# Performance work log

Measured on AMD Instinct MI355X. Metric: run time of the kernel, lower is better.

## Reference

```python
import jax, jax.numpy as jnp
import numpy as np

B, N, C = 64, 196, 768
H = 12
HD = C // H            # 64
TOPK = int(0.25 * HD)  # 16
HIDDEN = int(C * 4.0)  # 3072
SCALE = HD ** -0.5
EPS = 1e-5


def layernorm(x, g, b):
    mu = jnp.mean(x, axis=-1, keepdims=True)
    var = jnp.var(x, axis=-1, keepdims=True)
    return (x - mu) * jax.lax.rsqrt(var + EPS) * g + b


def setup_inputs() -> dict:
    key = jax.random.key(0)
    ks = jax.random.split(key, 8)
    s = 0.02
    return {
        "x": jax.random.normal(ks[0], (B, N, C), jnp.float32),
        "norm1_g": jnp.ones((C,), jnp.float32),
        "norm1_b": jnp.zeros((C,), jnp.float32),
        "qk_w": jax.random.normal(ks[1], (2 * C, C), jnp.float32) * s,   # torch Linear [out,in], no bias
        "attn_proj_w": jax.random.normal(ks[2], (C, H * TOPK), jnp.float32) * s,
        "attn_proj_b": jnp.zeros((C,), jnp.float32),
        "norm2_g": jnp.ones((C,), jnp.float32),
        "norm2_b": jnp.zeros((C,), jnp.float32),
        "fc1_w": jax.random.normal(ks[3], (HIDDEN, C), jnp.float32) * s,
        "fc1_b": jnp.zeros((HIDDEN,), jnp.float32),
        "fc2_w": jax.random.normal(ks[4], (C, HIDDEN), jnp.float32) * s,
        "fc2_b": jnp.zeros((C,), jnp.float32),
    }


def reference(x, norm1_g, norm1_b, qk_w, attn_proj_w, attn_proj_b,
              norm2_g, norm2_b, fc1_w, fc1_b, fc2_w, fc2_b):
    # --- HomoAttention branch ---
    h = layernorm(x, norm1_g, norm1_b)                       # [B,N,C]
    qk = h @ qk_w.T                                          # [B,N,2C]
    qk = qk.reshape(B, N, 2, H, HD).transpose(2, 0, 3, 1, 4) # [2,B,H,N,HD]
    q, k = qk[0] * SCALE, qk[1]
    attn = jnp.einsum('bhnd,bhmd->bhnm', q, k)               # [B,H,N,N]
    top_vals, _ = jax.lax.top_k(attn, TOPK)                  # [B,H,N,TOPK]
    a = jax.nn.softmax(top_vals, axis=-1)
    a = a.transpose(0, 2, 1, 3).reshape(B, N, H * TOPK)      # [B,N,H*TOPK]
    x = x + a @ attn_proj_w.T + attn_proj_b

    # --- MLP branch ---
    h2 = layernorm(x, norm2_g, norm2_b)
    h2 = jax.nn.gelu(h2 @ fc1_w.T + fc1_b, approximate=False)
    x = x + h2 @ fc2_w.T + fc2_b
    return x
```

## Files before the change

### kernel.cpp

```cpp
#include <hip/hip_runtime.h>


#define BATCH 64
#define SEQ   196
#define CH    768
#define NHEAD 12
#define HDIM  64
#define TOPK  16
#define HID   3072
#define MROWS 12544
#define MHALF 6272
#define SCALE_F 0.125f
#define NEGBIG -3e38f

typedef __bf16 bf16x8 __attribute__((ext_vector_type(8)));
typedef float  f32x4  __attribute__((ext_vector_type(4)));

__device__ __forceinline__ unsigned short f2b(float f) {
    union { float f; unsigned int i; } c; c.f = f;
    unsigned int u = c.i;
    return (unsigned short)((u + 0x7fffu + ((u >> 16) & 1u)) >> 16);
}
__device__ __forceinline__ float b2f(unsigned short u) {
    union { unsigned int i; float f; } c; c.i = ((unsigned int)u) << 16; return c.f;
}

__device__ __forceinline__ float gelu_f(float v) {
    float u = v * (0.7978845608f + 0.0356774081f * v * v);
    float e = __expf(2.0f * u);
    float th = 1.0f - 2.0f / (e + 1.0f);
    return 0.5f * v * (1.0f + th);
}

__device__ __forceinline__ void async16(const unsigned short* g, unsigned short* l) {
    __builtin_amdgcn_global_load_lds(
        (const __attribute__((address_space(1))) unsigned int*)(g),
        (__attribute__((address_space(3))) unsigned int*)(l), 16, 0, 0);
}

__global__ __launch_bounds__(256) void f2b4_k(const float* __restrict__ s0, unsigned short* __restrict__ d0, int n0,
                                              const float* __restrict__ s1, unsigned short* __restrict__ d1, int n1,
                                              const float* __restrict__ s2, unsigned short* __restrict__ d2, int n2,
                                              const float* __restrict__ s3, unsigned short* __restrict__ d3, int n3)
{
    int idx = (blockIdx.x * 256 + threadIdx.x) * 4;
    const float* s; unsigned short* d; int n;
    if (idx < n0) { s = s0; d = d0; n = n0; }
    else {
        idx -= n0;
        if (idx < n1) { s = s1; d = d1; n = n1; }
        else {
            idx -= n1;
            if (idx < n2) { s = s2; d = d2; n = n2; }
            else { idx -= n2; s = s3; d = d3; n = n3; }
        }
    }
    if (idx < n) {
        float4 v = *(const float4*)(s + idx);
        ushort4 o;
        o.x = f2b(v.x); o.y = f2b(v.y); o.z = f2b(v.z); o.w = f2b(v.w);
        *(ushort4*)(d + idx) = o;
    }
}

template<bool INF32>
__global__ __launch_bounds__(256) void ln_k(const void* __restrict__ xin,
                                            const float* __restrict__ gw,
                                            const float* __restrict__ bw,
                                            unsigned short* __restrict__ out)
{
    const int row = blockIdx.x;
    const int tid = threadIdx.x;
    float v0, v1, v2;
    if constexpr (INF32) {
        const float* xr = (const float*)xin + (size_t)row * CH;
        v0 = xr[tid]; v1 = xr[tid + 256]; v2 = xr[tid + 512];
    } else {
        const unsigned short* xr = (const unsigned short*)xin + (size_t)row * CH;
        v0 = b2f(xr[tid]); v1 = b2f(xr[tid + 256]); v2 = b2f(xr[tid + 512]);
    }
    float s  = v0 + v1 + v2;
    float sq = v0*v0 + v1*v1 + v2*v2;
#pragma unroll
    for (int off = 32; off > 0; off >>= 1) {
        s  += __shfl_down(s, off, 64);
        sq += __shfl_down(sq, off, 64);
    }
    __shared__ __align__(16) float red[8];
    if ((tid & 63) == 0) { red[(tid >> 6) * 2] = s; red[(tid >> 6) * 2 + 1] = sq; }
    __syncthreads();
    s  = red[0] + red[2] + red[4] + red[6];
    sq = red[1] + red[3] + red[5] + red[7];
    float mu  = s * (1.0f / CH);
    float var = sq * (1.0f / CH) - mu * mu;
    float rs  = rsqrtf(var + 1e-5f);
    unsigned short* orow = out + (size_t)row * CH;
    orow[tid]       = f2b((v0 - mu) * rs * gw[tid]       + bw[tid]);
    orow[tid + 256] = f2b((v1 - mu) * rs * gw[tid + 256] + bw[tid + 256]);
    orow[tid + 512] = f2b((v2 - mu) * rs * gw[tid + 512] + bw[tid + 512]);
}

template<int TM, int TN, bool BIAS, int RES, bool GELU, bool OUTF>
__global__ __launch_bounds__(256, 4)
void gemm_bt(const unsigned short* __restrict__ A,
             const unsigned short* __restrict__ Bw,
             const float* __restrict__ bias,
             const void* __restrict__ resid,
             void* __restrict__ Cout,
             int M, int N, int K)
{
    constexpr int WROWS = (TM == 128) ? 2 : 1;
    constexpr int WCOLS = 4 / WROWS;
    constexpr int JF = TN / (16 * WCOLS);
    __shared__ __align__(16) unsigned short As[2][TM * 32];
    __shared__ __align__(16) unsigned short Bs[2][TN * 32];
    const int tid  = threadIdx.x;
    const int w    = tid >> 6;
    const int lane = tid & 63;

    const int gridN = gridDim.x, gridM = gridDim.y;
    const int lid = blockIdx.y * gridN + blockIdx.x;
    const int SG = 8 * gridN;
    const int sg = lid / SG, r = lid % SG;
    const int remM = gridM - sg * 8;
    int mloc, nloc;
    if (remM >= 8) { mloc = sg * 8 + (r & 7); nloc = r >> 3; }
    else           { mloc = sg * 8 + r % remM; nloc = r / remM; }
    const int tileM = mloc * TM;
    const int tileN = nloc * TN;

    const int wm = (w / WCOLS) * 64;
    const int wn = (w % WCOLS) * (JF * 16);
    const int q   = lane >> 4;
    const int l16 = lane & 15;
    const int csw = (q ^ (l16 & 3)) * 8;

    f32x4 acc[4][JF];
#pragma unroll
    for (int i = 0; i < 4; ++i)
#pragma unroll
        for (int j = 0; j < JF; ++j) acc[i][j] = (f32x4){0.f, 0.f, 0.f, 0.f};

    const int r0 = tid >> 2;
    const int g0 = ((tid & 3) ^ (r0 & 3)) * 8;

    const unsigned short* pB[TN / 64];
    const unsigned short* pA[TM / 64];
#pragma unroll
    for (int c = 0; c < TN / 64; ++c) pB[c] = Bw + (size_t)(tileN + r0 + c * 64) * K + g0;
#pragma unroll
    for (int c = 0; c < TM / 64; ++c) pA[c] = A + (size_t)(tileM + r0 + c * 64) * K + g0;

    auto stage = [&](int buf) {
#pragma unroll
        for (int c = 0; c < TN / 64; ++c) {
            async16(pB[c], &Bs[buf][(size_t)(c * 256 + w * 64) * 8]);
            pB[c] += 32;
        }
#pragma unroll
        for (int c = 0; c < TM / 64; ++c) {
            async16(pA[c], &As[buf][(size_t)(c * 256 + w * 64) * 8]);
            pA[c] += 32;
        }
    };

    const int kIters = K >> 5;
    stage(0);
    int cur = 0;
    for (int kt = 0; kt < kIters; ++kt) {
        __syncthreads();
        if (kt + 1 < kIters) stage(cur ^ 1);
        bf16x8 af[4], bfr[JF];
#pragma unroll
        for (int i = 0; i < 4; ++i)
            af[i] = *(const bf16x8*)&As[cur][(wm + i * 16 + l16) * 32 + csw];
#pragma unroll
        for (int j = 0; j < JF; ++j)
            bfr[j] = *(const bf16x8*)&Bs[cur][(wn + j * 16 + l16) * 32 + csw];
#pragma unroll
        for (int i = 0; i < 4; ++i)
#pragma unroll
            for (int j = 0; j < JF; ++j)
                acc[i][j] = __builtin_amdgcn_mfma_f32_16x16x32_bf16(af[i], bfr[j], acc[i][j], 0, 0, 0);
        cur ^= 1;
    }

#pragma unroll
    for (int i = 0; i < 4; ++i) {
#pragma unroll
        for (int r2 = 0; r2 < 4; ++r2) {
            int row = tileM + wm + i * 16 + q * 4 + r2;
#pragma unroll
            for (int j = 0; j < JF; ++j) {
                int col = tileN + wn + j * 16 + l16;
                float v = acc[i][j][r2];
                if (BIAS) v += bias[col];
                if (GELU) v = gelu_f(v);
                if (RES == 1) v += ((const float*)resid)[(size_t)row * N + col];
                if (RES == 2) v += b2f(((const unsigned short*)resid)[(size_t)row * N + col]);
                if (OUTF) ((float*)Cout)[(size_t)row * N + col] = v;
                else      ((unsigned short*)Cout)[(size_t)row * N + col] = f2b(v);
            }
        }
    }
}

__global__ __launch_bounds__(256) void attn_topk(const unsigned short* __restrict__ qk,
                                                 unsigned short* __restrict__ aout)
{
    const int bh = blockIdx.x;
    const int b = bh / NHEAD, h = bh % NHEAD;
    __shared__ __align__(16) unsigned short Qs[208 * 64];
    __shared__ __align__(16) unsigned short Ks[208 * 64];
    const int tid = threadIdx.x;

    for (int i = tid; i < 208 * 8; i += 256) {
        int row = i >> 3, c = i & 7;
        uint4 vq = make_uint4(0, 0, 0, 0), vk = vq;
        if (row < SEQ) {
            const uint4* gp = (const uint4*)(qk + ((size_t)(b * SEQ + row) * 1536 + h * 64));
            vq = gp[c];
            vk = gp[c + 96];
        }
        int slot = c ^ (row & 7);
        *(uint4*)&Qs[row * 64 + slot * 8] = vq;
        *(uint4*)&Ks[row * 64 + slot * 8] = vk;
    }
    __syncthreads();

    const int w = tid >> 6, lane = tid & 63;
    const int q = lane >> 4, l16 = lane & 15;

    for (int tn = w; tn < 13; tn += 4) {
        const int nrow = tn * 16 + l16;
        const int nsw = nrow & 7;
        bf16x8 bq0 = *(const bf16x8*)&Qs[nrow * 64 + ((0 * 4 + q) ^ nsw) * 8];
        bf16x8 bq1 = *(const bf16x8*)&Qs[nrow * 64 + ((1 * 4 + q) ^ nsw) * 8];

        float t[TOPK];
#pragma unroll
        for (int j = 0; j < TOPK; ++j) t[j] = NEGBIG;

        for (int tm = 0; tm < 12; ++tm) {
            const int mrow = tm * 16 + l16;
            const int msw = mrow & 7;
            bf16x8 ak0 = *(const bf16x8*)&Ks[mrow * 64 + ((0 * 4 + q) ^ msw) * 8];
            bf16x8 ak1 = *(const bf16x8*)&Ks[mrow * 64 + ((1 * 4 + q) ^ msw) * 8];
            f32x4 acc = (f32x4){0.f, 0.f, 0.f, 0.f};
            acc = __builtin_amdgcn_mfma_f32_16x16x32_bf16(ak0, bq0, acc, 0, 0, 0);
            acc = __builtin_amdgcn_mfma_f32_16x16x32_bf16(ak1, bq1, acc, 0, 0, 0);
#pragma unroll
            for (int r = 0; r < 4; ++r) {
                float v = acc[r];
#pragma unroll
                for (int j = 0; j < TOPK; ++j) {
                    float mx = fmaxf(t[j], v);
                    v = fminf(t[j], v);
                    t[j] = mx;
                }
            }
        }
        {
            const int mrow = 12 * 16 + l16;
            const int msw = mrow & 7;
            bf16x8 ak0 = *(const bf16x8*)&Ks[mrow * 64 + ((0 * 4 + q) ^ msw) * 8];
            bf16x8 ak1 = *(const bf16x8*)&Ks[mrow * 64 + ((1 * 4 + q) ^ msw) * 8];
            f32x4 acc = (f32x4){0.f, 0.f, 0.f, 0.f};
            acc = __builtin_amdgcn_mfma_f32_16x16x32_bf16(ak0, bq0, acc, 0, 0, 0);
            acc = __builtin_amdgcn_mfma_f32_16x16x32_bf16(ak1, bq1, acc, 0, 0, 0);
#pragma unroll
            for (int r = 0; r < 4; ++r) {
                float v = (q == 0) ? acc[r] : NEGBIG;
#pragma unroll
                for (int j = 0; j < TOPK; ++j) {
                    float mx = fmaxf(t[j], v);
                    v = fminf(t[j], v);
                    t[j] = mx;
                }
            }
        }

#pragma unroll
        for (int stage = 0; stage < 2; ++stage) {
            const int xm = 16 << stage;
            float bl[TOPK], c[TOPK];
#pragma unroll
            for (int j = 0; j < TOPK; ++j) bl[j] = __shfl_xor(t[j], xm, 64);
#pragma unroll
            for (int j = 0; j < TOPK; ++j) c[j] = fmaxf(t[j], bl[TOPK - 1 - j]);
#pragma unroll
            for (int s = 8; s >= 1; s >>= 1) {
#pragma unroll
                for (int i = 0; i < TOPK; ++i) {
                    if ((i & s) == 0) {
                        float mx = fmaxf(c[i], c[i + s]);
                        c[i + s] = fminf(c[i], c[i + s]);
                        c[i] = mx;
                    }
                }
            }
#pragma unroll
            for (int j = 0; j < TOPK; ++j) t[j] = c[j];
        }

        if (q == 0 && nrow < SEQ) {
            float e[TOPK], sum = 0.f;
#pragma unroll
            for (int j = 0; j < TOPK; ++j) { e[j] = __expf((t[j] - t[0]) * SCALE_F); sum += e[j]; }
            float inv = 1.0f / sum;
            unsigned int pk[8];
#pragma unroll
            for (int jj = 0; jj < 8; ++jj)
                pk[jj] = (unsigned int)f2b(e[2 * jj] * inv) |
                         ((unsigned int)f2b(e[2 * jj + 1] * inv) << 16);
            unsigned short* dst = aout + ((size_t)(b * SEQ + nrow)) * (NHEAD * TOPK) + h * TOPK;
            ((uint4*)dst)[0] = make_uint4(pk[0], pk[1], pk[2], pk[3]);
            ((uint4*)dst)[1] = make_uint4(pk[4], pk[5], pk[6], pk[7]);
        }
    }
}

extern "C" void kernel_launch(void* const* d_in, const int* in_sizes, int n_in,
                              void* d_out, int out_size, void* d_ws, size_t ws_size,
                              hipStream_t stream)
{
    const float* x    = (const float*)d_in[0];
    const float* g1   = (const float*)d_in[1];
    const float* bb1  = (const float*)d_in[2];
    const float* qkw  = (const float*)d_in[3];
    const float* pw   = (const float*)d_in[4];
    const float* pb   = (const float*)d_in[5];
    const float* g2   = (const float*)d_in[6];
    const float* bb2  = (const float*)d_in[7];
    const float* f1w  = (const float*)d_in[8];
    const float* f1b  = (const float*)d_in[9];
    const float* f2w  = (const float*)d_in[10];
    const float* f2bp = (const float*)d_in[11];
    float* out = (float*)d_out;

    char* ws = (char*)d_ws;
    const size_t SZ_H   = (size_t)MROWS * CH * 2;
    const size_t N_WQK  = (size_t)2 * CH * CH;
    const size_t N_WP   = (size_t)CH * (NHEAD * TOPK);
    const size_t N_WF   = (size_t)HID * CH;
    const size_t SZ_W   = (N_WQK + N_WP + 2 * N_WF) * 2;
    const size_t SZ_A   = (size_t)MROWS * (NHEAD * TOPK) * 2;
    const size_t SZ_QK  = (size_t)MROWS * 2 * CH * 2;
    const size_t SZ_GGF = (size_t)MROWS * HID * 2;

    unsigned short* hbuf = (unsigned short*)(ws);
    unsigned short* wqk  = (unsigned short*)(ws + SZ_H);
    unsigned short* wp   = wqk + N_WQK;
    unsigned short* wf1  = wp  + N_WP;
    unsigned short* wf2  = wf1 + N_WF;
    unsigned short* av   = (unsigned short*)(ws + SZ_H + SZ_W);
    unsigned short* qk   = (unsigned short*)(ws + SZ_H + SZ_W + SZ_A);
    unsigned short* gg   = qk;

    const size_t base = SZ_H + SZ_W + SZ_A;
    const bool fullMLP = ws_size >= base + SZ_GGF + SZ_H;
    const bool bx1     = fullMLP || ws_size >= base + SZ_QK + SZ_H;
    unsigned short* x1b = (unsigned short*)(ws + base + (fullMLP ? SZ_GGF : SZ_QK));
    float* x1 = out;

    {
        int total4 = (int)((N_WQK + N_WP + 2 * N_WF) / 4);
        f2b4_k<<<(total4 + 255) / 256, 256, 0, stream>>>(
            qkw, wqk, (int)N_WQK, pw, wp, (int)N_WP,
            f1w, wf1, (int)N_WF, f2w, wf2, (int)N_WF);
    }

    ln_k<true><<<MROWS, 256, 0, stream>>>(x, g1, bb1, hbuf);
    gemm_bt<128, 128, false, 0, false, false><<<dim3(12, 98), 256, 0, stream>>>(
        hbuf, wqk, nullptr, nullptr, qk, MROWS, 2*CH, CH);
    attn_topk<<<BATCH * NHEAD, 256, 0, stream>>>(qk, av);

    if (bx1) {
        gemm_bt<64, 128, true, 1, false, false><<<dim3(6, 196), 256, 0, stream>>>(
            av, wp, pb, x, x1b, MROWS, CH, NHEAD*TOPK);
        ln_k<false><<<MROWS, 256, 0, stream>>>(x1b, g2, bb2, hbuf);
        if (fullMLP) {
            gemm_bt<128, 128, true, 0, true, false><<<dim3(24, 98), 256, 0, stream>>>(
                hbuf, wf1, f1b, nullptr, gg, MROWS, HID, CH);
            gemm_bt<64, 256, true, 2, false, true><<<dim3(3, 196), 256, 0, stream>>>(
                gg, wf2, f2bp, x1b, out, MROWS, CH, HID);
        } else {
            for (int half = 0; half < 2; ++half) {
                const size_t ro = (size_t)half * MHALF;
                gemm_bt<128, 128, true, 0, true, false><<<dim3(24, 49), 256, 0, stream>>>(
                    hbuf + ro * CH, wf1, f1b, nullptr, gg, MHALF, HID, CH);
                gemm_bt<64, 256, true, 2, false, true><<<dim3(3, 98), 256, 0, stream>>>(
                    gg, wf2, f2bp, x1b + ro * CH, out + ro * CH, MHALF, CH, HID);
            }
        }
    } else {
        gemm_bt<64, 128, true, 1, false, true><<<dim3(6, 196), 256, 0, stream>>>(
            av, wp, pb, x, x1, MROWS, CH, NHEAD*TOPK);
        ln_k<true><<<MROWS, 256, 0, stream>>>(x1, g2, bb2, hbuf);
        for (int half = 0; half < 2; ++half) {
            const size_t ro = (size_t)half * MHALF;
            gemm_bt<128, 128, true, 0, true, false><<<dim3(24, 49), 256, 0, stream>>>(
                hbuf + ro * CH, wf1, f1b, nullptr, gg, MHALF, HID, CH);
            gemm_bt<64, 256, true, 1, false, true><<<dim3(3, 98), 256, 0, stream>>>(
                gg, wf2, f2bp, x1 + ro * CH, out + ro * CH, MHALF, CH, HID);
        }
    }
}
```

Baseline: 438.6 us.

## Add 256x256 eight-wave pipelined GEMM for QK, FC1 and FC2 projections

Introduces a new bf16 MFMA GEMM kernel with 256x256 output tiles, 512 threads, double-buffered async global-to-LDS staging split into quarter stages interleaved with MFMA phases, setprio hints, and a grouped tile ordering for L2 reuse. It replaces the 128x128 and 64x256 GEMMs for the QK projection and both MLP GEMMs on the full-workspace path. The larger tiles cut global traffic per FLOP. In exchange, register and LDS use rise, and there are fewer tiles to spread across the compute units. MROWS=12544 divides evenly by 256 (49 tiles), so no bounds checks are needed.

Result: slower. 448.6 us (+2.3%).

```diff
diff --git a/kernel.cpp b/kernel.cpp
--- a/kernel.cpp
+++ b/kernel.cpp
@@ -205,6 +205,178 @@
     }
 }
 
+template<int KC, bool BIAS, int RES, bool GELU, bool OUTF>
+__global__ __launch_bounds__(512, 2)
+void gemm8p(const unsigned short* __restrict__ A,
+            const unsigned short* __restrict__ Bw,
+            const float* __restrict__ bias,
+            const void* __restrict__ resid,
+            void* __restrict__ Cout,
+            int M, int N)
+{
+    constexpr int T = KC / 64;
+    __shared__ __align__(16) unsigned short As[2][256 * 64];
+    __shared__ __align__(16) unsigned short Bs[2][256 * 64];
+    const int tid  = threadIdx.x;
+    const int w    = tid >> 6;
+    const int lane = tid & 63;
+    const int q    = lane >> 4;
+    const int l16  = lane & 15;
+
+    const int gridN = gridDim.x, gridM = gridDim.y;
+    const int lid = blockIdx.y * gridN + blockIdx.x;
+    const int SG = 8 * gridN;
+    const int sg = lid / SG, rr = lid % SG;
+    const int remM = gridM - sg * 8;
+    int mloc, nloc;
+    if (remM >= 8) { mloc = sg * 8 + (rr & 7); nloc = rr >> 3; }
+    else           { mloc = sg * 8 + rr % remM; nloc = rr / remM; }
+    const int tileM = mloc * 256, tileN = nloc * 256;
+
+    const int wm = (w >> 2) * 128;
+    const int wn = (w & 3) * 64;
+
+    const int r0 = tid >> 3;
+    const int g0 = (tid & 7) ^ (r0 & 7);
+    const unsigned short* pA0 = A  + (size_t)(tileM + r0) * KC + g0 * 8;
+    const unsigned short* pB0 = Bw + (size_t)(tileN + r0) * KC + g0 * 8;
+
+    auto stageHT = [&](int v, int j) {
+        const unsigned short* src = (j < 2 ? pA0 : pB0)
+                                  + (size_t)(j & 1) * 128 * KC + (size_t)v * 64;
+        unsigned short* dst = (j < 2 ? As[v & 1] : Bs[v & 1]) + (j & 1) * 8192 + w * 512;
+        async16(src, dst);
+        async16(src + (size_t)64 * KC, dst + 4096);
+    };
+
+    f32x4 acc[8][4];
+#pragma unroll
+    for (int i = 0; i < 8; ++i)
+#pragma unroll
+        for (int jn = 0; jn < 4; ++jn) acc[i][jn] = (f32x4){0.f, 0.f, 0.f, 0.f};
+
+    stageHT(0, 0); stageHT(0, 1); stageHT(0, 2); stageHT(0, 3); stageHT(1, 0);
+    asm volatile("s_waitcnt vmcnt(2)" ::: "memory");
+    __builtin_amdgcn_s_barrier();
+
+    const int arow = wm + l16;
+    const int brow = wn + l16;
+    const int xsw  = l16 & 7;
+
+#pragma unroll 2
+    for (int u = 0; u < T; ++u) {
+        const unsigned short* Ab = As[u & 1];
+        const unsigned short* Bb = Bs[u & 1];
+        bf16x8 af[4][2], b0[2][2], b1[2][2];
+
+#pragma unroll
+        for (int m = 0; m < 4; ++m)
+#pragma unroll
+            for (int kk = 0; kk < 2; ++kk)
+                af[m][kk] = *(const bf16x8*)&Ab[(arow + m * 16) * 64 + ((((kk << 2) | q) ^ xsw) << 3)];
+#pragma unroll
+        for (int n = 0; n < 2; ++n)
+#pragma unroll
+            for (int kk = 0; kk < 2; ++kk)
+                b0[n][kk] = *(const bf16x8*)&Bb[(brow + n * 16) * 64 + ((((kk << 2) | q) ^ xsw) << 3)];
+        if (u + 1 < T) stageHT(u + 1, 1);
+        __builtin_amdgcn_s_barrier();
+        asm volatile("s_waitcnt lgkmcnt(0)" ::: "memory");
+        __builtin_amdgcn_sched_barrier(0);
+        __builtin_amdgcn_s_setprio(1);
+#pragma unroll
+        for (int kk = 0; kk < 2; ++kk)
+#pragma unroll
+            for (int m = 0; m < 4; ++m)
+#pragma unroll
+                for (int n = 0; n < 2; ++n)
+                    acc[m][n] = __builtin_amdgcn_mfma_f32_16x16x32_bf16(af[m][kk], b0[n][kk], acc[m][n], 0, 0, 0);
+        __builtin_amdgcn_s_setprio(0);
+        __builtin_amdgcn_s_barrier();
+
+#pragma unroll
+        for (int n = 0; n < 2; ++n)
+#pragma unroll
+            for (int kk = 0; kk < 2; ++kk)
+                b1[n][kk] = *(const bf16x8*)&Bb[(brow + 32 + n * 16) * 64 + ((((kk << 2) | q) ^ xsw) << 3)];
+        if (u + 1 < T) stageHT(u + 1, 2);
+        __builtin_amdgcn_s_barrier();
+        asm volatile("s_waitcnt lgkmcnt(0)" ::: "memory");
+        __builtin_amdgcn_sched_barrier(0);
+        __builtin_amdgcn_s_setprio(1);
+#pragma unroll
+        for (int kk = 0; kk < 2; ++kk)
+#pragma unroll
+            for (int m = 0; m < 4; ++m)
+#pragma unroll
+                for (int n = 0; n < 2; ++n)
+                    acc[m][2 + n] = __builtin_amdgcn_mfma_f32_16x16x32_bf16(af[m][kk], b1[n][kk], acc[m][2 + n], 0, 0, 0);
+        __builtin_amdgcn_s_setprio(0);
+        __builtin_amdgcn_s_barrier();
+
+#pragma unroll
+        for (int m = 0; m < 4; ++m)
+#pragma unroll
+            for (int kk = 0; kk < 2; ++kk)
+                af[m][kk] = *(const bf16x8*)&Ab[(arow + 64 + m * 16) * 64 + ((((kk << 2) | q) ^ xsw) << 3)];
+        if (u + 1 < T) stageHT(u + 1, 3);
+        __builtin_amdgcn_s_barrier();
+        asm volatile("s_waitcnt lgkmcnt(0)" ::: "memory");
+        __builtin_amdgcn_sched_barrier(0);
+        __builtin_amdgcn_s_setprio(1);
+#pragma unroll
+        for (int kk = 0; kk < 2; ++kk)
+#pragma unroll
+            for (int m = 0; m < 4; ++m)
+#pragma unroll
+                for (int n = 0; n < 2; ++n)
+                    acc[4 + m][2 + n] = __builtin_amdgcn_mfma_f32_16x16x32_bf16(af[m][kk], b1[n][kk], acc[4 + m][2 + n], 0, 0, 0);
+        __builtin_amdgcn_s_setprio(0);
+        __builtin_amdgcn_s_barrier();
+
+        if (u + 2 < T) {
+            stageHT(u + 2, 0);
+            asm volatile("s_waitcnt vmcnt(2)" ::: "memory");
+        } else if (u + 1 < T) {
+            asm volatile("s_waitcnt vmcnt(0)" ::: "memory");
+        }
+        __builtin_amdgcn_s_barrier();
+        __builtin_amdgcn_s_setprio(1);
+#pragma unroll
+        for (int kk = 0; kk < 2; ++kk)
+#pragma unroll
+            for (int m = 0; m < 4; ++m)
+#pragma unroll
+                for (int n = 0; n < 2; ++n)
+                    acc[4 + m][n] = __builtin_amdgcn_mfma_f32_16x16x32_bf16(af[m][kk], b0[n][kk], acc[4 + m][n], 0, 0, 0);
+        __builtin_amdgcn_s_setprio(0);
+        __builtin_amdgcn_s_barrier();
+    }
+
+#pragma unroll
+    for (int mh = 0; mh < 2; ++mh)
+#pragma unroll
+        for (int m = 0; m < 4; ++m)
+#pragma unroll
+            for (int r2 = 0; r2 < 4; ++r2) {
+                const int row = tileM + wm + mh * 64 + m * 16 + q * 4 + r2;
+#pragma unroll
+                for (int nh = 0; nh < 2; ++nh)
+#pragma unroll
+                    for (int n = 0; n < 2; ++n) {
+                        const int col = tileN + wn + nh * 32 + n * 16 + l16;
+                        float v = acc[mh * 4 + m][nh * 2 + n][r2];
+                        if (BIAS) v += bias[col];
+                        if (GELU) v = gelu_f(v);
+                        if (RES == 1) v += ((const float*)resid)[(size_t)row * N + col];
+                        if (RES == 2) v += b2f(((const unsigned short*)resid)[(size_t)row * N + col]);
+                        if (OUTF) ((float*)Cout)[(size_t)row * N + col] = v;
+                        else      ((unsigned short*)Cout)[(size_t)row * N + col] = f2b(v);
+                    }
+            }
+    (void)M;
+}
+
 __global__ __launch_bounds__(256) void attn_topk(const unsigned short* __restrict__ qk,
                                                  unsigned short* __restrict__ aout)
 {
@@ -371,19 +543,19 @@
     }
 
     ln_k<true><<<MROWS, 256, 0, stream>>>(x, g1, bb1, hbuf);
-    gemm_bt<128, 128, false, 0, false, false><<<dim3(12, 98), 256, 0, stream>>>(
-        hbuf, wqk, nullptr, nullptr, qk, MROWS, 2*CH, CH);
+    gemm8p<CH, false, 0, false, false><<<dim3(2 * CH / 256, MROWS / 256), 512, 0, stream>>>(
+        hbuf, wqk, nullptr, nullptr, qk, MROWS, 2 * CH);
     attn_topk<<<BATCH * NHEAD, 256, 0, stream>>>(qk, av);
 
     if (bx1) {
         gemm_bt<64, 128, true, 1, false, false><<<dim3(6, 196), 256, 0, stream>>>(
-            av, wp, pb, x, x1b, MROWS, CH, NHEAD*TOPK);
+            av, wp, pb, x, x1b, MROWS, CH, NHEAD * TOPK);
         ln_k<false><<<MROWS, 256, 0, stream>>>(x1b, g2, bb2, hbuf);
         if (fullMLP) {
-            gemm_bt<128, 128, true, 0, true, false><<<dim3(24, 98), 256, 0, stream>>>(
-                hbuf, wf1, f1b, nullptr, gg, MROWS, HID, CH);
-            gemm_bt<64, 256, true, 2, false, true><<<dim3(3, 196), 256, 0, stream>>>(
-                gg, wf2, f2bp, x1b, out, MROWS, CH, HID);
+            gemm8p<CH, true, 0, true, false><<<dim3(HID / 256, MROWS / 256), 512, 0, stream>>>(
+                hbuf, wf1, f1b, nullptr, gg, MROWS, HID);
+            gemm8p<HID, true, 2, false, true><<<dim3(CH / 256, MROWS / 256), 512, 0, stream>>>(
+                gg, wf2, f2bp, x1b, out, MROWS, CH);
         } else {
             for (int half = 0; half < 2; ++half) {
                 const size_t ro = (size_t)half * MHALF;
@@ -395,7 +567,7 @@
         }
     } else {
         gemm_bt<64, 128, true, 1, false, true><<<dim3(6, 196), 256, 0, stream>>>(
-            av, wp, pb, x, x1, MROWS, CH, NHEAD*TOPK);
+            av, wp, pb, x, x1, MROWS, CH, NHEAD * TOPK);
         ln_k<true><<<MROWS, 256, 0, stream>>>(x1, g2, bb2, hbuf);
         for (int half = 0; half < 2; ++half) {
             const size_t ro = (size_t)half * MHALF;
```

## Replace GEMMs with persistent 128x256 tile kernel using LDS-staged vector epilogue

Applied to the files above, without the earlier changes.

Adds a persistent GEMM kernel launched with 768 blocks of 512 threads. Each block walks 128x256 output tiles in an order grouped by M so blocks share weight panels, with double-buffered async loads over K-slices of 32. The epilogue stages each wave's results in shared memory so global stores are 16-byte vectors. It replaces the QK, projection, FC1 and FC2 GEMMs on the main path, aiming for better B reuse, fewer launches' worth of tail effects and more coalesced writes. It assumes M is a multiple of 128 and N a multiple of 256, and uses larger shared-memory buffers that may lower occupancy.

New measurement: 433.4 us. About the same (-1.2%).

```diff
diff --git a/kernel.cpp b/kernel.cpp
--- a/kernel.cpp
+++ b/kernel.cpp
@@ -205,6 +205,159 @@
     }
 }
 
+template<bool BIAS, int RES, bool GELU, bool OUTF>
+__global__ __launch_bounds__(512, 4)
+void gemm_p(const unsigned short* __restrict__ A,
+            const unsigned short* __restrict__ Bw,
+            const float* __restrict__ bias,
+            const void* __restrict__ resid,
+            void* __restrict__ Cout,
+            int M, int N, int K)
+{
+    __shared__ __align__(16) unsigned short As[2][128 * 32];
+    __shared__ __align__(16) unsigned short Bs[2][256 * 32];
+    const int tid  = threadIdx.x;
+    const int w    = tid >> 6;
+    const int lane = tid & 63;
+    const int q    = lane >> 4;
+    const int l16  = lane & 15;
+
+    const int gridM = M >> 7, gridN = N >> 8;
+    const int P = gridDim.x;
+
+    const int x   = (int)blockIdx.x & 7;
+    const int bj  = (int)blockIdx.x >> 3;
+    const int Bx  = (P >> 3) + (((P & 7) > x) ? 1 : 0);
+    const int cnt = (gridM - x + 7) >> 3;
+    const int ntx = cnt * gridN;
+
+    const int wm = (w >> 2) * 64;
+    const int wn = (w & 3) * 64;
+    const int r0 = tid >> 2;
+    const int g0 = ((tid & 3) ^ (r0 & 3)) * 8;
+    const int csw = (q ^ (l16 & 3)) * 8;
+
+    for (int t = bj; t < ntx; t += Bx) {
+        const int nn = t / cnt, ii = t - nn * cnt;
+        const int tileM = (x + (ii << 3)) << 7;
+        const int tileN = nn << 8;
+
+        __syncthreads();
+
+        const unsigned short* pA  = A  + (size_t)(tileM + r0) * K + g0;
+        const unsigned short* pB0 = Bw + (size_t)(tileN + r0) * K + g0;
+        const unsigned short* pB1 = Bw + (size_t)(tileN + 128 + r0) * K + g0;
+
+        f32x4 acc[4][4];
+#pragma unroll
+        for (int i = 0; i < 4; ++i)
+#pragma unroll
+            for (int j = 0; j < 4; ++j) acc[i][j] = (f32x4){0.f, 0.f, 0.f, 0.f};
+
+        auto stage = [&](int buf) {
+            async16(pB0, &Bs[buf][(size_t)w * 512]);        pB0 += 32;
+            async16(pB1, &Bs[buf][4096 + (size_t)w * 512]); pB1 += 32;
+            async16(pA,  &As[buf][(size_t)w * 512]);        pA  += 32;
+        };
+
+        const int kIters = K >> 5;
+        stage(0);
+        int cur = 0;
+        for (int kt = 0; kt < kIters; ++kt) {
+            __syncthreads();
+            if (kt + 1 < kIters) stage(cur ^ 1);
+            bf16x8 af[4], bf[4];
+#pragma unroll
+            for (int i = 0; i < 4; ++i)
+                af[i] = *(const bf16x8*)&As[cur][(wm + i * 16 + l16) * 32 + csw];
+#pragma unroll
+            for (int j = 0; j < 4; ++j)
+                bf[j] = *(const bf16x8*)&Bs[cur][(wn + j * 16 + l16) * 32 + csw];
+#pragma unroll
+            for (int i = 0; i < 4; ++i)
+#pragma unroll
+                for (int j = 0; j < 4; ++j)
+                    acc[i][j] = __builtin_amdgcn_mfma_f32_16x16x32_bf16(af[i], bf[j], acc[i][j], 0, 0, 0);
+            cur ^= 1;
+        }
+
+        __syncthreads();
+
+        float bsh[4];
+        if (BIAS) {
+#pragma unroll
+            for (int j = 0; j < 4; ++j) bsh[j] = bias[tileN + wn + j * 16 + l16];
+        }
+
+        if constexpr (!OUTF) {
+            unsigned short* slab = &Bs[0][0] + (size_t)w * 1152;
+            unsigned short* co = (unsigned short*)Cout;
+#pragma unroll
+            for (int i = 0; i < 4; ++i) {
+#pragma unroll
+                for (int j = 0; j < 4; ++j)
+#pragma unroll
+                    for (int r2 = 0; r2 < 4; ++r2) {
+                        float v = acc[i][j][r2];
+                        if (BIAS) v += bsh[j];
+                        if (GELU) v = gelu_f(v);
+                        slab[(q * 4 + r2) * 72 + j * 16 + l16] = f2b(v);
+                    }
+#pragma unroll
+                for (int h = 0; h < 2; ++h) {
+                    const int lr = h * 8 + (lane >> 3);
+                    const int grow = tileM + wm + i * 16 + lr;
+                    const int gcol = tileN + wn + (lane & 7) * 8;
+                    uint4 pk = *(const uint4*)&slab[lr * 72 + (lane & 7) * 8];
+                    if (RES != 0) {
+                        unsigned short* ps = (unsigned short*)&pk;
+#pragma unroll
+                        for (int jj = 0; jj < 8; ++jj) {
+                            float v = b2f(ps[jj]);
+                            if (RES == 1) v += ((const float*)resid)[(size_t)grow * N + gcol + jj];
+                            if (RES == 2) v += b2f(((const unsigned short*)resid)[(size_t)grow * N + gcol + jj]);
+                            ps[jj] = f2b(v);
+                        }
+                    }
+                    *(uint4*)&co[(size_t)grow * N + gcol] = pk;
+                }
+            }
+        } else {
+            float* slabf = (w == 7) ? (float*)&As[0][0]
+                                    : (float*)&Bs[0][0] + (size_t)w * 1088;
+            float* co = (float*)Cout;
+#pragma unroll
+            for (int i = 0; i < 4; ++i) {
+#pragma unroll
+                for (int j = 0; j < 4; ++j)
+#pragma unroll
+                    for (int r2 = 0; r2 < 4; ++r2) {
+                        float v = acc[i][j][r2];
+                        if (BIAS) v += bsh[j];
+                        if (GELU) v = gelu_f(v);
+                        slabf[(q * 4 + r2) * 68 + j * 16 + l16] = v;
+                    }
+#pragma unroll
+                for (int i4 = 0; i4 < 4; ++i4) {
+                    const int lr = i4 * 4 + (lane >> 4);
+                    const int grow = tileM + wm + i * 16 + lr;
+                    const int gcol = tileN + wn + (lane & 15) * 4;
+                    f32x4 vv = *(const f32x4*)&slabf[lr * 68 + (lane & 15) * 4];
+                    if (RES == 1) {
+                        const float4 r4 = *(const float4*)&((const float*)resid)[(size_t)grow * N + gcol];
+                        vv[0] += r4.x; vv[1] += r4.y; vv[2] += r4.z; vv[3] += r4.w;
+                    }
+                    if (RES == 2) {
+                        const ushort4 r4 = *(const ushort4*)&((const unsigned short*)resid)[(size_t)grow * N + gcol];
+                        vv[0] += b2f(r4.x); vv[1] += b2f(r4.y); vv[2] += b2f(r4.z); vv[3] += b2f(r4.w);
+                    }
+                    *(f32x4*)&co[(size_t)grow * N + gcol] = vv;
+                }
+            }
+        }
+    }
+}
+
 __global__ __launch_bounds__(256) void attn_topk(const unsigned short* __restrict__ qk,
                                                  unsigned short* __restrict__ aout)
 {
@@ -371,18 +524,18 @@
     }
 
     ln_k<true><<<MROWS, 256, 0, stream>>>(x, g1, bb1, hbuf);
-    gemm_bt<128, 128, false, 0, false, false><<<dim3(12, 98), 256, 0, stream>>>(
-        hbuf, wqk, nullptr, nullptr, qk, MROWS, 2*CH, CH);
+    gemm_p<false, 0, false, false><<<768, 512, 0, stream>>>(
+        hbuf, wqk, nullptr, nullptr, qk, MROWS, 2 * CH, CH);
     attn_topk<<<BATCH * NHEAD, 256, 0, stream>>>(qk, av);
 
     if (bx1) {
-        gemm_bt<64, 128, true, 1, false, false><<<dim3(6, 196), 256, 0, stream>>>(
-            av, wp, pb, x, x1b, MROWS, CH, NHEAD*TOPK);
+        gemm_p<true, 1, false, false><<<768, 512, 0, stream>>>(
+            av, wp, pb, x, x1b, MROWS, CH, NHEAD * TOPK);
         ln_k<false><<<MROWS, 256, 0, stream>>>(x1b, g2, bb2, hbuf);
         if (fullMLP) {
-            gemm_bt<128, 128, true, 0, true, false><<<dim3(24, 98), 256, 0, stream>>>(
+            gemm_p<true, 0, true, false><<<768, 512, 0, stream>>>(
                 hbuf, wf1, f1b, nullptr, gg, MROWS, HID, CH);
-            gemm_bt<64, 256, true, 2, false, true><<<dim3(3, 196), 256, 0, stream>>>(
+            gemm_p<true, 2, false, true><<<768, 512, 0, stream>>>(
                 gg, wf2, f2bp, x1b, out, MROWS, CH, HID);
         } else {
             for (int half = 0; half < 2; ++half) {
@@ -395,7 +548,7 @@
         }
     } else {
         gemm_bt<64, 128, true, 1, false, true><<<dim3(6, 196), 256, 0, stream>>>(
-            av, wp, pb, x, x1, MROWS, CH, NHEAD*TOPK);
+            av, wp, pb, x, x1, MROWS, CH, NHEAD * TOPK);
         ln_k<true><<<MROWS, 256, 0, stream>>>(x1, g2, bb2, hbuf);
         for (int half = 0; half < 2; ++half) {
             const size_t ro = (size_t)half * MHALF;
```
